# Performance work log

Measured on AMD Instinct MI355X. Metric: run time of the kernel, lower is better.

The kernel has to match this reference:

```python
import jax, jax.numpy as jnp
import numpy as np

N_NODES = 50000
N_EDGES = 800000
D_IN = 256
D_HID = 256
N_CLASSES = 32
N_GRAPHS = 64


def _sage_conv(x, src, dst, W_l, b_l, W_r, num_nodes):
    # PyG SAGEConv (mean aggr, root_weight=True):
    # out = lin_l(mean_{j->i} x_j) + lin_r(x_i)
    msg = x[src]                                                   # [E, d]
    agg = jax.ops.segment_sum(msg, dst, num_segments=num_nodes)   # [N, d]
    cnt = jax.ops.segment_sum(jnp.ones((src.shape[0], 1), x.dtype), dst,
                              num_segments=num_nodes)             # [N, 1]
    agg = agg / jnp.maximum(cnt, 1.0)
    return agg @ W_l + b_l + x @ W_r


def setup_inputs() -> dict:
    key = jax.random.key(0)
    ks = jax.random.split(key, 12)
    x = jax.random.normal(ks[0], (N_NODES, D_IN), dtype=jnp.float32)
    edge_index = jax.random.randint(ks[1], (2, N_EDGES), 0, N_NODES, dtype=jnp.int64)
    batch = jnp.sort(jax.random.randint(ks[2], (N_NODES,), 0, N_GRAPHS, dtype=jnp.int64))
    s1 = 1.0 / np.sqrt(D_IN)
    s2 = 1.0 / np.sqrt(D_HID)
    return {
        "x": x,
        "edge_index": edge_index,
        "batch": batch,
        "W1_l": jax.random.uniform(ks[3], (D_IN, D_HID), jnp.float32, -s1, s1),
        "b1": jax.random.uniform(ks[4], (D_HID,), jnp.float32, -s1, s1),
        "W1_r": jax.random.uniform(ks[5], (D_IN, D_HID), jnp.float32, -s1, s1),
        "W2_l": jax.random.uniform(ks[6], (D_HID, D_HID), jnp.float32, -s2, s2),
        "b2": jax.random.uniform(ks[7], (D_HID,), jnp.float32, -s2, s2),
        "W2_r": jax.random.uniform(ks[8], (D_HID, D_HID), jnp.float32, -s2, s2),
        "Wc": jax.random.uniform(ks[9], (D_HID, N_CLASSES), jnp.float32, -s2, s2),
        "bc": jax.random.uniform(ks[10], (N_CLASSES,), jnp.float32, -s2, s2),
    }


def reference(x, edge_index, batch, W1_l, b1, W1_r, W2_l, b2, W2_r, Wc, bc):
    src, dst = edge_index[0], edge_index[1]
    h = jax.nn.relu(_sage_conv(x, src, dst, W1_l, b1, W1_r, N_NODES))
    h = jax.nn.relu(_sage_conv(h, src, dst, W2_l, b2, W2_r, N_NODES))
    # global mean pool over graphs
    gsum = jax.ops.segment_sum(h, batch, num_segments=N_GRAPHS)        # [G, d]
    gcnt = jax.ops.segment_sum(jnp.ones((h.shape[0], 1), h.dtype), batch,
                               num_segments=N_GRAPHS)                  # [G, 1]
    g = gsum / jnp.maximum(gcnt, 1.0)
    return g @ Wc + bc
```

## Files before the change

### kernel.cpp

```cpp
#include <hip/hip_runtime.h>
#include <stdint.h>

#define NNODES 50000
#define NEDGES 800000
#define DDIM 256
#define NCLS 32
#define NGRAPH 64
#define NSCANB ((NNODES + 255) / 256)

typedef short bf16x8 __attribute__((ext_vector_type(8)));
typedef float f32x4 __attribute__((ext_vector_type(4)));
typedef unsigned short u16x8 __attribute__((ext_vector_type(8)));

typedef __attribute__((address_space(1))) const char glb_c;
typedef __attribute__((address_space(3))) char lds_c;

__device__ __forceinline__ unsigned short f2b(float f) {
  uint32_t u = __builtin_bit_cast(uint32_t, f);
  u += 0x7FFFu + ((u >> 16) & 1u);
  return (unsigned short)(u >> 16);
}
__device__ __forceinline__ float b2f(unsigned short u) {
  return __builtin_bit_cast(float, (uint32_t)u << 16);
}

__device__ __forceinline__ void gload16(const void* g, const void* l) {
  __builtin_amdgcn_global_load_lds((glb_c*)g, (lds_c*)l, 16, 0, 0);
}


__global__ void k_hist(const int* __restrict__ dst, int* __restrict__ cnt) {
  int e = blockIdx.x * 256 + threadIdx.x;
  if (e < NEDGES) atomicAdd(&cnt[dst[e]], 1);
}

__global__ void k_scan1(const int* __restrict__ cnt, int* __restrict__ bsum) {
  int b = blockIdx.x;
  int i = b * 256 + threadIdx.x;
  int lane = threadIdx.x & 63, wid = threadIdx.x >> 6;
  int v = (i < NNODES) ? cnt[i] : 0;
#pragma unroll
  for (int o = 1; o < 64; o <<= 1) v += __shfl_xor(v, o, 64);
  __shared__ int ws[4];
  if (lane == 0) ws[wid] = v;
  __syncthreads();
  if (threadIdx.x == 0) bsum[b] = ws[0] + ws[1] + ws[2] + ws[3];
}

__global__ void k_scan2(const int* __restrict__ bsum, int* __restrict__ boffs) {
  int tid = threadIdx.x, lane = tid & 63, wid = tid >> 6;
  int v = (tid < NSCANB) ? bsum[tid] : 0;
  int s = v;
#pragma unroll
  for (int o = 1; o < 64; o <<= 1) {
    int t = __shfl_up(s, o, 64);
    if (lane >= o) s += t;
  }
  __shared__ int ws[4];
  if (lane == 63) ws[wid] = s;
  __syncthreads();
  int add = 0;
  for (int w = 0; w < wid; ++w) add += ws[w];
  if (tid < NSCANB) boffs[tid] = s + add - v;
}

__global__ void k_scan3(const int* __restrict__ cnt, const int* __restrict__ boffs,
                        int* __restrict__ rowptr, int* __restrict__ cursor) {
  int b = blockIdx.x;
  int i = b * 256 + threadIdx.x;
  int lane = threadIdx.x & 63, wid = threadIdx.x >> 6;
  int v = (i < NNODES) ? cnt[i] : 0;
  int s = v;
#pragma unroll
  for (int o = 1; o < 64; o <<= 1) {
    int t = __shfl_up(s, o, 64);
    if (lane >= o) s += t;
  }
  __shared__ int ws[4];
  if (lane == 63) ws[wid] = s;
  __syncthreads();
  int add = boffs[b];
  for (int w = 0; w < wid; ++w) add += ws[w];
  int incl = s + add;
  if (i < NNODES) {
    rowptr[i + 1] = incl;
    cursor[i] = incl - v;
  }
  if (b == 0 && threadIdx.x == 0) rowptr[0] = 0;
}

__global__ void k_fill(const int* __restrict__ src, const int* __restrict__ dst,
                       int* __restrict__ cursor, int* __restrict__ col) {
  int e = blockIdx.x * 256 + threadIdx.x;
  if (e < NEDGES) {
    int p = atomicAdd(&cursor[dst[e]], 1);
    col[p] = src[e];
  }
}


__global__ void k_cvt_x(const float* __restrict__ x, unsigned short* __restrict__ xb) {
  int i = blockIdx.x * 256 + threadIdx.x;
  if (i < NNODES * DDIM / 4) {
    float4 v = ((const float4*)x)[i];
    ushort4 o;
    o.x = f2b(v.x); o.y = f2b(v.y); o.z = f2b(v.z); o.w = f2b(v.w);
    ((ushort4*)xb)[i] = o;
  }
}

__global__ void k_cvt_w(const float* __restrict__ W1l, const float* __restrict__ W1r,
                        const float* __restrict__ W2l, const float* __restrict__ W2r,
                        unsigned short* __restrict__ WT1, unsigned short* __restrict__ WT2) {
  int idx = blockIdx.x * 256 + threadIdx.x;
  int which = idx >> 17;
  int id2 = idx & 131071;
  int n = id2 >> 9, k = id2 & 511;
  const float* Wl = which ? W2l : W1l;
  const float* Wr = which ? W2r : W1r;
  unsigned short* WT = which ? WT2 : WT1;
  float v = (k < 256) ? Wl[k * 256 + n] : Wr[(k - 256) * 256 + n];
  WT[id2] = f2b(v);
}


__global__ void k_agg(const unsigned short* __restrict__ feat,
                      const int* __restrict__ rowptr, const int* __restrict__ col,
                      unsigned short* __restrict__ out) {
  int node = (blockIdx.x << 2) + (threadIdx.x >> 6);
  if (node >= NNODES) return;
  int lane = threadIdx.x & 63;
  int half = lane >> 5;
  int seg = lane & 31;
  int s = rowptr[node], e = rowptr[node + 1];
  float a[8] = {0.f, 0.f, 0.f, 0.f, 0.f, 0.f, 0.f, 0.f};
  int i = s;
  for (; i + 4 <= e; i += 4) {
    int c0 = col[i + half];
    int c1 = col[i + 2 + half];
    u16x8 v0 = *(const u16x8*)(feat + (size_t)c0 * DDIM + seg * 8);
    u16x8 v1 = *(const u16x8*)(feat + (size_t)c1 * DDIM + seg * 8);
#pragma unroll
    for (int j = 0; j < 8; ++j) a[j] += b2f(v0[j]) + b2f(v1[j]);
  }
  for (; i < e; i += 2) {
    int idx = i + half;
    if (idx < e) {
      u16x8 v = *(const u16x8*)(feat + (size_t)col[idx] * DDIM + seg * 8);
#pragma unroll
      for (int j = 0; j < 8; ++j) a[j] += b2f(v[j]);
    }
  }
#pragma unroll
  for (int j = 0; j < 8; ++j) a[j] += __shfl_xor(a[j], 32, 64);
  if (half == 0) {
    float inv = (e > s) ? 1.f / (float)(e - s) : 0.f;
    u16x8 o;
#pragma unroll
    for (int j = 0; j < 8; ++j) o[j] = f2b(a[j] * inv);
    *(u16x8*)(out + (size_t)node * DDIM + seg * 8) = o;
  }
}


__global__ void k_gemm(const unsigned short* __restrict__ Aagg,
                       const unsigned short* __restrict__ Aroot,
                       const unsigned short* __restrict__ WT,
                       const float* __restrict__ bias,
                       unsigned short* __restrict__ out) {
  __shared__ unsigned short As[128 * 32];
  __shared__ unsigned short Bs[128 * 32];
  int m0 = blockIdx.x * 128;
  int n0 = blockIdx.y * 128;
  int tid = threadIdx.x, lane = tid & 63, wv = tid >> 6;
  int wm = wv >> 1, wn = wv & 1;

  f32x4 acc[4][4];
#pragma unroll
  for (int m = 0; m < 4; ++m)
#pragma unroll
    for (int n = 0; n < 4; ++n) acc[m][n] = (f32x4)0.f;

  for (int kt = 0; kt < 16; ++kt) {
    int k = kt * 32;
    const unsigned short* Abase = (k < 256) ? Aagg : Aroot;
    int kk = k & 255;
#pragma unroll
    for (int q = 0; q < 2; ++q) {
      int idx = q * 256 + tid;
      int row = idx >> 2, seg = idx & 3;
      int gr = m0 + row;
      if (gr >= NNODES) gr = NNODES - 1;
      const unsigned short* sp = Abase + (size_t)gr * DDIM + kk + seg * 8;
      gload16(sp, (const char*)As + (q * 256 + wv * 64) * 16);
    }
#pragma unroll
    for (int q = 0; q < 2; ++q) {
      int idx = q * 256 + tid;
      int row = idx >> 2, seg = idx & 3;
      const unsigned short* sp = WT + (size_t)(n0 + row) * 512 + k + seg * 8;
      gload16(sp, (const char*)Bs + (q * 256 + wv * 64) * 16);
    }
    __syncthreads();

    bf16x8 af[4], bfr[4];
    int kb = (lane >> 4) * 8;
    int rA = wm * 64 + (lane & 15);
    int rB = wn * 64 + (lane & 15);
#pragma unroll
    for (int m = 0; m < 4; ++m) af[m] = *(const bf16x8*)&As[(rA + m * 16) * 32 + kb];
#pragma unroll
    for (int n = 0; n < 4; ++n) bfr[n] = *(const bf16x8*)&Bs[(rB + n * 16) * 32 + kb];
#pragma unroll
    for (int m = 0; m < 4; ++m)
#pragma unroll
      for (int n = 0; n < 4; ++n)
        acc[m][n] = __builtin_amdgcn_mfma_f32_16x16x32_bf16(af[m], bfr[n], acc[m][n], 0, 0, 0);
    __syncthreads();
  }

  int rbase = m0 + wm * 64 + (lane >> 4) * 4;
  int cbase = n0 + wn * 64 + (lane & 15);
#pragma unroll
  for (int n = 0; n < 4; ++n) {
    int cc = cbase + n * 16;
    float bv = bias[cc];
#pragma unroll
    for (int m = 0; m < 4; ++m) {
#pragma unroll
      for (int j = 0; j < 4; ++j) {
        int r = rbase + m * 16 + j;
        if (r < NNODES) {
          float v = acc[m][n][j] + bv;
          v = fmaxf(v, 0.f);
          out[(size_t)r * DDIM + cc] = f2b(v);
        }
      }
    }
  }
}


__global__ void k_cnt(const int* __restrict__ batch, int* __restrict__ cnt) {
  int g = threadIdx.x;
  if (g >= NGRAPH) return;
  int lo = 0, hi = NNODES;
  while (lo < hi) { int m = (lo + hi) >> 1; if (batch[m] < g) lo = m + 1; else hi = m; }
  int lo2 = lo, hi2 = NNODES;
  while (lo2 < hi2) { int m = (lo2 + hi2) >> 1; if (batch[m] < g + 1) lo2 = m + 1; else hi2 = m; }
  cnt[g] = lo2 - lo;
}

#define GSUM_WAVES 1024
__global__ void k_gsum(const unsigned short* __restrict__ h2,
                       const int* __restrict__ batch,
                       float* __restrict__ gsum) {
  int wave = (blockIdx.x * blockDim.x + threadIdx.x) >> 6;
  int lane = threadIdx.x & 63;
  const int per = (NNODES + GSUM_WAVES - 1) / GSUM_WAVES;
  int r0 = wave * per;
  int r1 = r0 + per; if (r1 > NNODES) r1 = NNODES;
  if (r0 >= r1) return;
  float a0 = 0.f, a1 = 0.f, a2 = 0.f, a3 = 0.f;
  int cur = batch[r0];
  for (int r = r0; r < r1; ++r) {
    int g = batch[r];
    if (g != cur) {
      float* gp = gsum + cur * DDIM + lane * 4;
      atomicAdd(gp + 0, a0); atomicAdd(gp + 1, a1);
      atomicAdd(gp + 2, a2); atomicAdd(gp + 3, a3);
      a0 = a1 = a2 = a3 = 0.f;
      cur = g;
    }
    ushort4 v = *(const ushort4*)(h2 + (size_t)r * DDIM + lane * 4);
    a0 += b2f(v.x); a1 += b2f(v.y); a2 += b2f(v.z); a3 += b2f(v.w);
  }
  float* gp = gsum + cur * DDIM + lane * 4;
  atomicAdd(gp + 0, a0); atomicAdd(gp + 1, a1);
  atomicAdd(gp + 2, a2); atomicAdd(gp + 3, a3);
}

__global__ void k_cls(const float* __restrict__ gsum, const int* __restrict__ cnt,
                      const float* __restrict__ Wc, const float* __restrict__ bc,
                      float* __restrict__ out) {
  int g = blockIdx.x;
  __shared__ float colmean[DDIM];
  int c = threadIdx.x;
  int n = cnt[g];
  float inv = (n > 0) ? 1.f / (float)n : 0.f;
  colmean[c] = gsum[g * DDIM + c] * inv;
  __syncthreads();
  if (c < NCLS) {
    float o = bc[c];
#pragma unroll 4
    for (int k = 0; k < DDIM; ++k) o += colmean[k] * Wc[k * NCLS + c];
    out[g * NCLS + c] = o;
  }
}


extern "C" void kernel_launch(void* const* d_in, const int* in_sizes, int n_in,
                              void* d_out, int out_size, void* d_ws, size_t ws_size,
                              hipStream_t stream) {
  const float* x    = (const float*)d_in[0];
  const int* eidx   = (const int*)d_in[1];
  const int* batch  = (const int*)d_in[2];
  const float* W1l  = (const float*)d_in[3];
  const float* b1   = (const float*)d_in[4];
  const float* W1r  = (const float*)d_in[5];
  const float* W2l  = (const float*)d_in[6];
  const float* b2   = (const float*)d_in[7];
  const float* W2r  = (const float*)d_in[8];
  const float* Wc   = (const float*)d_in[9];
  const float* bc   = (const float*)d_in[10];
  float* out = (float*)d_out;

  const int* esrc = eidx;
  const int* edst = eidx + NEDGES;

  char* w = (char*)d_ws;
  size_t off = 0;
  auto alloc = [&](size_t bytes) -> char* {
    char* p = w + off;
    off = (off + bytes + 255) & ~(size_t)255;
    return p;
  };
  int* rowptr = (int*)alloc((NNODES + 1) * sizeof(int));
  int* cursor = (int*)alloc(NNODES * sizeof(int));
  int* col    = (int*)alloc(NEDGES * sizeof(int));
  unsigned short* xb   = (unsigned short*)alloc((size_t)NNODES * DDIM * 2);
  unsigned short* h1b  = (unsigned short*)alloc((size_t)NNODES * DDIM * 2);
  unsigned short* aggb = (unsigned short*)alloc((size_t)NNODES * DDIM * 2);
  unsigned short* WT1  = (unsigned short*)alloc(512 * 256 * 2);
  unsigned short* WT2  = (unsigned short*)alloc(512 * 256 * 2);
  float* gsum = (float*)alloc(NGRAPH * DDIM * sizeof(float));
  int* gcnt   = (int*)alloc(NGRAPH * sizeof(int));
  int* bsum   = (int*)alloc(NSCANB * sizeof(int));
  int* boffs  = (int*)alloc(NSCANB * sizeof(int));

  hipMemsetAsync(cursor, 0, NNODES * sizeof(int), stream);
  k_hist<<<(NEDGES + 255) / 256, 256, 0, stream>>>(edst, cursor);
  k_scan1<<<NSCANB, 256, 0, stream>>>(cursor, bsum);
  k_scan2<<<1, 256, 0, stream>>>(bsum, boffs);
  k_scan3<<<NSCANB, 256, 0, stream>>>(cursor, boffs, rowptr, cursor);
  k_fill<<<(NEDGES + 255) / 256, 256, 0, stream>>>(esrc, edst, cursor, col);

  k_cvt_x<<<(NNODES * DDIM / 4 + 255) / 256, 256, 0, stream>>>(x, xb);
  k_cvt_w<<<(2 * 256 * 512 + 255) / 256, 256, 0, stream>>>(W1l, W1r, W2l, W2r, WT1, WT2);

  dim3 ggrid((NNODES + 127) / 128, 2);

  k_agg<<<(NNODES + 3) / 4, 256, 0, stream>>>(xb, rowptr, col, aggb);
  k_gemm<<<ggrid, 256, 0, stream>>>(aggb, xb, WT1, b1, h1b);

  k_agg<<<(NNODES + 3) / 4, 256, 0, stream>>>(h1b, rowptr, col, aggb);
  k_gemm<<<ggrid, 256, 0, stream>>>(aggb, h1b, WT2, b2, xb);

  hipMemsetAsync(gsum, 0, NGRAPH * DDIM * sizeof(float), stream);
  k_cnt<<<1, 64, 0, stream>>>(batch, gcnt);
  k_gsum<<<GSUM_WAVES / 4, 256, 0, stream>>>(xb, batch, gsum);
  k_cls<<<NGRAPH, 256, 0, stream>>>(gsum, gcnt, Wc, bc, out);
}
```

Baseline: 345.3 us.

## Store node features in 32-column slabs so aggregation gathers stay cache-resident

Node feature matrices are changed from row-major [N,256] to eight column slabs of [N,32] bf16. The conversion, GEMM loads and stores, and pooling kernels are all updated to match. The aggregation kernel now assigns one slab per block (blockIdx&7), so each pass gathers only a 3.2 MB slab, which should fit in cache and cut random-gather traffic to HBM. In exchange, each node's edge list is re-read eight times, per-gather accesses shrink to 8-byte loads, and the GEMM epilogue writes land with a stride of 64 bytes.

```diff
diff --git a/kernel.cpp b/kernel.cpp
--- a/kernel.cpp
+++ b/kernel.cpp
@@ -11,9 +11,11 @@
 typedef short bf16x8 __attribute__((ext_vector_type(8)));
 typedef float f32x4 __attribute__((ext_vector_type(4)));
 typedef unsigned short u16x8 __attribute__((ext_vector_type(8)));
+typedef unsigned short u16x4 __attribute__((ext_vector_type(4)));
 
 typedef __attribute__((address_space(1))) const char glb_c;
 typedef __attribute__((address_space(3))) char lds_c;
+
 
 __device__ __forceinline__ unsigned short f2b(float f) {
   uint32_t u = __builtin_bit_cast(uint32_t, f);
@@ -101,11 +103,13 @@
 
 __global__ void k_cvt_x(const float* __restrict__ x, unsigned short* __restrict__ xb) {
   int i = blockIdx.x * 256 + threadIdx.x;
-  if (i < NNODES * DDIM / 4) {
-    float4 v = ((const float4*)x)[i];
-    ushort4 o;
+  if (i < NNODES * 64) {
+    int r = i >> 6, c4 = i & 63;
+    float4 v = *(const float4*)(x + (size_t)r * DDIM + c4 * 4);
+    u16x4 o;
     o.x = f2b(v.x); o.y = f2b(v.y); o.z = f2b(v.z); o.w = f2b(v.w);
-    ((ushort4*)xb)[i] = o;
+    int slab = c4 >> 3, seg = c4 & 7;
+    *(u16x4*)(xb + ((size_t)slab * NNODES + r) * 32 + seg * 4) = o;
   }
 }
 
@@ -127,38 +131,37 @@
 __global__ void k_agg(const unsigned short* __restrict__ feat,
                       const int* __restrict__ rowptr, const int* __restrict__ col,
                       unsigned short* __restrict__ out) {
-  int node = (blockIdx.x << 2) + (threadIdx.x >> 6);
+  int g = blockIdx.x & 7;
+  int nb = blockIdx.x >> 3;
+  int wv = threadIdx.x >> 6, lane = threadIdx.x & 63;
+  int node = nb * 8 + wv;
   if (node >= NNODES) return;
-  int lane = threadIdx.x & 63;
-  int half = lane >> 5;
-  int seg = lane & 31;
+  int es = lane >> 3;
+  int seg = lane & 7;
+  const unsigned short* slab = feat + (size_t)g * NNODES * 32;
   int s = rowptr[node], e = rowptr[node + 1];
-  float a[8] = {0.f, 0.f, 0.f, 0.f, 0.f, 0.f, 0.f, 0.f};
-  int i = s;
-  for (; i + 4 <= e; i += 4) {
-    int c0 = col[i + half];
-    int c1 = col[i + 2 + half];
-    u16x8 v0 = *(const u16x8*)(feat + (size_t)c0 * DDIM + seg * 8);
-    u16x8 v1 = *(const u16x8*)(feat + (size_t)c1 * DDIM + seg * 8);
-#pragma unroll
-    for (int j = 0; j < 8; ++j) a[j] += b2f(v0[j]) + b2f(v1[j]);
-  }
-  for (; i < e; i += 2) {
-    int idx = i + half;
+  float a0 = 0.f, a1 = 0.f, a2 = 0.f, a3 = 0.f;
+  for (int i = s; i < e; i += 8) {
+    int idx = i + es;
     if (idx < e) {
-      u16x8 v = *(const u16x8*)(feat + (size_t)col[idx] * DDIM + seg * 8);
-#pragma unroll
-      for (int j = 0; j < 8; ++j) a[j] += b2f(v[j]);
-    }
-  }
-#pragma unroll
-  for (int j = 0; j < 8; ++j) a[j] += __shfl_xor(a[j], 32, 64);
-  if (half == 0) {
+      int ce = __builtin_nontemporal_load(col + idx);
+      u16x4 v = *(const u16x4*)(slab + (size_t)ce * 32 + seg * 4);
+      a0 += b2f(v.x); a1 += b2f(v.y); a2 += b2f(v.z); a3 += b2f(v.w);
+    }
+  }
+#pragma unroll
+  for (int o = 8; o < 64; o <<= 1) {
+    a0 += __shfl_xor(a0, o, 64);
+    a1 += __shfl_xor(a1, o, 64);
+    a2 += __shfl_xor(a2, o, 64);
+    a3 += __shfl_xor(a3, o, 64);
+  }
+  if (es == 0) {
     float inv = (e > s) ? 1.f / (float)(e - s) : 0.f;
-    u16x8 o;
-#pragma unroll
-    for (int j = 0; j < 8; ++j) o[j] = f2b(a[j] * inv);
-    *(u16x8*)(out + (size_t)node * DDIM + seg * 8) = o;
+    u16x4 o;
+    o.x = f2b(a0 * inv); o.y = f2b(a1 * inv); o.z = f2b(a2 * inv); o.w = f2b(a3 * inv);
+    unsigned short* op = out + ((size_t)g * NNODES + node) * 32 + seg * 4;
+    __builtin_nontemporal_store(o, (u16x4*)op);
   }
 }
 
@@ -184,14 +187,15 @@
   for (int kt = 0; kt < 16; ++kt) {
     int k = kt * 32;
     const unsigned short* Abase = (k < 256) ? Aagg : Aroot;
-    int kk = k & 255;
+    int slab = (k & 255) >> 5;
+    const unsigned short* Aslab = Abase + (size_t)slab * NNODES * 32;
 #pragma unroll
     for (int q = 0; q < 2; ++q) {
       int idx = q * 256 + tid;
       int row = idx >> 2, seg = idx & 3;
       int gr = m0 + row;
       if (gr >= NNODES) gr = NNODES - 1;
-      const unsigned short* sp = Abase + (size_t)gr * DDIM + kk + seg * 8;
+      const unsigned short* sp = Aslab + (size_t)gr * 32 + seg * 8;
       gload16(sp, (const char*)As + (q * 256 + wv * 64) * 16);
     }
 #pragma unroll
@@ -225,6 +229,7 @@
   for (int n = 0; n < 4; ++n) {
     int cc = cbase + n * 16;
     float bv = bias[cc];
+    size_t sbase = (size_t)(cc >> 5) * NNODES * 32 + (cc & 31);
 #pragma unroll
     for (int m = 0; m < 4; ++m) {
 #pragma unroll
@@ -233,7 +238,7 @@
         if (r < NNODES) {
           float v = acc[m][n][j] + bv;
           v = fmaxf(v, 0.f);
-          out[(size_t)r * DDIM + cc] = f2b(v);
+          out[sbase + (size_t)r * 32] = f2b(v);
         }
       }
     }
@@ -261,21 +266,24 @@
   int r0 = wave * per;
   int r1 = r0 + per; if (r1 > NNODES) r1 = NNODES;
   if (r0 >= r1) return;
+  int slab = lane >> 3, seg = lane & 7;
+  int cb = slab * 32 + seg * 4;
+  const unsigned short* sp = h2 + (size_t)slab * NNODES * 32 + seg * 4;
   float a0 = 0.f, a1 = 0.f, a2 = 0.f, a3 = 0.f;
   int cur = batch[r0];
   for (int r = r0; r < r1; ++r) {
     int g = batch[r];
     if (g != cur) {
-      float* gp = gsum + cur * DDIM + lane * 4;
+      float* gp = gsum + cur * DDIM + cb;
       atomicAdd(gp + 0, a0); atomicAdd(gp + 1, a1);
       atomicAdd(gp + 2, a2); atomicAdd(gp + 3, a3);
       a0 = a1 = a2 = a3 = 0.f;
       cur = g;
     }
-    ushort4 v = *(const ushort4*)(h2 + (size_t)r * DDIM + lane * 4);
+    u16x4 v = *(const u16x4*)(sp + (size_t)r * 32);
     a0 += b2f(v.x); a1 += b2f(v.y); a2 += b2f(v.z); a3 += b2f(v.w);
   }
-  float* gp = gsum + cur * DDIM + lane * 4;
+  float* gp = gsum + cur * DDIM + cb;
   atomicAdd(gp + 0, a0); atomicAdd(gp + 1, a1);
   atomicAdd(gp + 2, a2); atomicAdd(gp + 3, a3);
 }
@@ -345,15 +353,16 @@
   k_scan3<<<NSCANB, 256, 0, stream>>>(cursor, boffs, rowptr, cursor);
   k_fill<<<(NEDGES + 255) / 256, 256, 0, stream>>>(esrc, edst, cursor, col);
 
-  k_cvt_x<<<(NNODES * DDIM / 4 + 255) / 256, 256, 0, stream>>>(x, xb);
+  k_cvt_x<<<(NNODES * 64 + 255) / 256, 256, 0, stream>>>(x, xb);
   k_cvt_w<<<(2 * 256 * 512 + 255) / 256, 256, 0, stream>>>(W1l, W1r, W2l, W2r, WT1, WT2);
 
   dim3 ggrid((NNODES + 127) / 128, 2);
-
-  k_agg<<<(NNODES + 3) / 4, 256, 0, stream>>>(xb, rowptr, col, aggb);
+  int agg_grid = (NNODES / 8) * 8;
+
+  k_agg<<<agg_grid, 512, 0, stream>>>(xb, rowptr, col, aggb);
   k_gemm<<<ggrid, 256, 0, stream>>>(aggb, xb, WT1, b1, h1b);
 
-  k_agg<<<(NNODES + 3) / 4, 256, 0, stream>>>(h1b, rowptr, col, aggb);
+  k_agg<<<agg_grid, 512, 0, stream>>>(h1b, rowptr, col, aggb);
   k_gemm<<<ggrid, 256, 0, stream>>>(aggb, h1b, WT2, b2, xb);
 
   hipMemsetAsync(gsum, 0, NGRAPH * DDIM * sizeof(float), stream);
```

Result: slower. 519.2 us (+50.4%).
